# Kernel optimization log

Hardware: AMD Instinct MI355X
Metric: run time of the kernel (lower is better)

## Reference

```python
import jax, jax.numpy as jnp
import numpy as np

VOCAB, D, PAD, SPARSITY = 6, 32, 5, 0.15


def setup_inputs() -> dict:
    key = jax.random.key(0)
    ks = jax.random.split(key, 16)
    x = jax.random.randint(ks[0], (256, 4096), 0, VOCAB, dtype=jnp.int32)
    s = 0.1
    emb = jax.random.normal(ks[1], (VOCAB, D), jnp.float32) * s
    return {
        "x": x,
        "emb": emb,
        # selector: D -> D//2 -> 1 (sigmoid)
        "sel_w1": jax.random.normal(ks[2], (D, D // 2), jnp.float32) * s,
        "sel_b1": jnp.zeros((D // 2,), jnp.float32),
        "sel_w2": jax.random.normal(ks[3], (D // 2, 1), jnp.float32) * s,
        "sel_b2": jnp.zeros((1,), jnp.float32),
        # approximator: D -> D -> D
        "app_w1": jax.random.normal(ks[4], (D, D), jnp.float32) * s,
        "app_b1": jnp.zeros((D,), jnp.float32),
        "app_w2": jax.random.normal(ks[5], (D, D), jnp.float32) * s,
        "app_b2": jnp.zeros((D,), jnp.float32),
        # classifier: D -> D//2 -> 1 (sigmoid)
        "cls_w1": jax.random.normal(ks[6], (D, D // 2), jnp.float32) * s,
        "cls_b1": jnp.zeros((D // 2,), jnp.float32),
        "cls_w2": jax.random.normal(ks[7], (D // 2, 1), jnp.float32) * s,
        "cls_b2": jnp.zeros((1,), jnp.float32),
    }


def reference(x, emb, sel_w1, sel_b1, sel_w2, sel_b2,
              app_w1, app_b1, app_w2, app_b2,
              cls_w1, cls_b1, cls_w2, cls_b2):
    B, S = x.shape
    k = max(1, int(S * SPARSITY))
    table = emb.at[PAD].set(0.0)            # padding_idx row is zero
    e = table[x]                            # [B, S, D]
    # selector scores (tiny MLP + sigmoid)
    h = jax.nn.relu(e @ sel_w1 + sel_b1)
    scores = jax.nn.sigmoid((h @ sel_w2 + sel_b2).squeeze(-1))  # [B, S]
    _, top_idx = jax.lax.top_k(scores, k)   # [B, k]
    sel = jnp.take_along_axis(e, top_idx[..., None], axis=1)    # [B, k, D]
    a = jax.nn.relu(sel @ app_w1 + app_b1) @ app_w2 + app_b2    # [B, k, D]
    pooled = a.mean(axis=1)                 # [B, D]
    c = jax.nn.relu(pooled @ cls_w1 + cls_b1)
    pred = jax.nn.sigmoid((c @ cls_w2 + cls_b2).squeeze(-1))    # [B]
    return pred, top_idx, scores
```

## Files before the change

kernel.cpp:

```cpp
#include <hip/hip_runtime.h>
#include <math.h>

#define VOCABN 6
#define DIM 32
#define PADI 5
#define BATCH 256
#define SEQ 4096
#define KSEL 614

__device__ __forceinline__ int mbcnt64(unsigned long long m) {
    return __builtin_amdgcn_mbcnt_hi((unsigned)(m >> 32),
           __builtin_amdgcn_mbcnt_lo((unsigned)m, 0u));
}

__device__ __forceinline__ float lut6(float s0, float s1, float s2, float s3,
                                      float s4, float s5, int tk) {
    float r = s0;
    r = (tk == 1) ? s1 : r;
    r = (tk == 2) ? s2 : r;
    r = (tk == 3) ? s3 : r;
    r = (tk == 4) ? s4 : r;
    r = (tk == 5) ? s5 : r;
    return r;
}

__global__ __launch_bounds__(1024) void fused_row_kernel(
    const int* __restrict__ x,
    const float* __restrict__ emb,
    const float* __restrict__ sel_w1, const float* __restrict__ sel_b1,
    const float* __restrict__ sel_w2, const float* __restrict__ sel_b2,
    const float* __restrict__ app_w1, const float* __restrict__ app_b1,
    const float* __restrict__ app_w2, const float* __restrict__ app_b2,
    const float* __restrict__ cls_w1, const float* __restrict__ cls_b1,
    const float* __restrict__ cls_w2, const float* __restrict__ cls_b2,
    float* __restrict__ out_pred,
    float* __restrict__ out_topidx,
    float* __restrict__ out_scores) {
    const int b = blockIdx.x;
    const int t = threadIdx.x;
    const int lane = t & 63;
    const int w = t >> 6;

    __shared__ float s_emb[VOCABN * DIM];
    __shared__ float s_selw1[DIM * (DIM / 2)];
    __shared__ float s_selb1[DIM / 2], s_selw2[DIM / 2];
    __shared__ float s_selb2, s_clsb2v;
    __shared__ float s_appw1[DIM * DIM];
    __shared__ float s_appw2[DIM * DIM];
    __shared__ float s_appb1[DIM], s_appb2[DIM];
    __shared__ float s_clsw1[DIM * (DIM / 2)];
    __shared__ float s_clsb1[DIM / 2], s_clsw2[DIM / 2];
    __shared__ float s_ah[VOCABN * DIM];
    __shared__ __align__(16) float s_score[8];
    __shared__ __align__(16) int s_wtot[16][8];
    __shared__ __align__(16) int s_wpre[16][8];
    __shared__ __align__(16) int s_selbase[8];

    const int4 tw = *(const int4*)(x + (size_t)b * SEQ + t * 4);

    s_appw1[t] = app_w1[t];
    s_appw2[t] = app_w2[t];
    if (t < 512) s_selw1[t] = sel_w1[t];
    else s_clsw1[t - 512] = cls_w1[t - 512];
    if (t < 192) s_emb[t] = (t >= PADI * DIM) ? 0.f : emb[t];
    else if (t < 208) { int i = t - 192; s_selb1[i] = sel_b1[i]; }
    else if (t < 224) { int i = t - 208; s_selw2[i] = sel_w2[i]; }
    else if (t < 256) { int i = t - 224; s_appb1[i] = app_b1[i]; }
    else if (t < 288) { int i = t - 256; s_appb2[i] = app_b2[i]; }
    else if (t < 304) { int i = t - 288; s_clsb1[i] = cls_b1[i]; }
    else if (t < 320) { int i = t - 304; s_clsw2[i] = cls_w2[i]; }
    else if (t == 320) s_selb2 = sel_b2[0];
    else if (t == 321) s_clsb2v = cls_b2[0];

    int tok[4];
    tok[0] = tw.x; tok[1] = tw.y; tok[2] = tw.z; tok[3] = tw.w;

    unsigned long long msk[VOCABN][4];
    #pragma unroll
    for (int v = 0; v < VOCABN; ++v) {
        #pragma unroll
        for (int i = 0; i < 4; ++i) msk[v][i] = __ballot(tok[i] == v);
    }
    if (lane == 0) {
        int c[VOCABN];
        #pragma unroll
        for (int v = 0; v < VOCABN; ++v)
            c[v] = __popcll(msk[v][0]) + __popcll(msk[v][1]) +
                   __popcll(msk[v][2]) + __popcll(msk[v][3]);
        *(int4*)&s_wtot[w][0] = make_int4(c[0], c[1], c[2], c[3]);
        *(int2*)&s_wtot[w][4] = make_int2(c[4], c[5]);
    }

    __syncthreads();

    if (w == 0) {
        int sv = lane >> 3; if (sv >= VOCABN) sv -= VOCABN;
        const int j0 = (lane & 7) * 2;
        const float2 bj = *(const float2*)(s_selb1 + j0);
        const float2 wj = *(const float2*)(s_selw2 + j0);
        float h0 = bj.x, h1 = bj.y;
        #pragma unroll
        for (int d = 0; d < DIM; ++d) {
            const float e = s_emb[sv * DIM + d];
            const float2 ww = *(const float2*)(s_selw1 + d * (DIM / 2) + j0);
            h0 += e * ww.x;
            h1 += e * ww.y;
        }
        float part = fmaxf(h0, 0.f) * wj.x + fmaxf(h1, 0.f) * wj.y;
        part += __shfl_xor(part, 1, 64);
        part += __shfl_xor(part, 2, 64);
        part += __shfl_xor(part, 4, 64);
        const float sig = 1.f / (1.f + expf(-(part + s_selb2)));
        float scv[VOCABN];
        #pragma unroll
        for (int v = 0; v < VOCABN; ++v) scv[v] = __shfl(sig, v * 8, 64);
        if (lane < VOCABN) s_score[lane] = scv[lane];

        int tv[VOCABN];
        #pragma unroll
        for (int v = 0; v < VOCABN; ++v) tv[v] = s_wtot[lane & 15][v];
        #pragma unroll
        for (int m = 1; m <= 8; m <<= 1) {
            #pragma unroll
            for (int v = 0; v < VOCABN; ++v) tv[v] += __shfl_xor(tv[v], m, 64);
        }
        int rk[VOCABN];
        #pragma unroll
        for (int v = 0; v < VOCABN; ++v) {
            int r = 0;
            #pragma unroll
            for (int u = 0; u < VOCABN; ++u) {
                if (scv[u] > scv[v]) ++r;
                else if (scv[u] == scv[v] && u < v) ++r;
            }
            rk[v] = r;
        }
        if (lane < VOCABN) {
            const int v = lane;
            int before = 0;
            #pragma unroll
            for (int u = 0; u < VOCABN; ++u) before += (rk[u] < rk[v]) ? tv[u] : 0;
            const int base = before < KSEL ? before : KSEL;
            int take = KSEL - base;
            take = tv[v] < take ? tv[v] : take;
            take = take > 0 ? take : 0;
            s_selbase[v] = take | (base << 16);
        }
    } else if (w == 1) {
        int tv[VOCABN], inc[VOCABN];
        #pragma unroll
        for (int v = 0; v < VOCABN; ++v) { tv[v] = s_wtot[lane & 15][v]; inc[v] = tv[v]; }
        #pragma unroll
        for (int off = 1; off <= 8; off <<= 1) {
            #pragma unroll
            for (int v = 0; v < VOCABN; ++v) {
                int up = __shfl_up(inc[v], off, 64);
                if ((lane & 15) >= off) inc[v] += up;
            }
        }
        if (lane < 16) {
            *(int4*)&s_wpre[lane][0] = make_int4(inc[0] - tv[0], inc[1] - tv[1],
                                                 inc[2] - tv[2], inc[3] - tv[3]);
            *(int2*)&s_wpre[lane][4] = make_int2(inc[4] - tv[4], inc[5] - tv[5]);
        }
    } else if (w >= 2 && w < 5) {
        const int i = t - 128, v = i >> 5, j = i & 31;
        float acc = s_appb1[j];
        #pragma unroll
        for (int d = 0; d < DIM; ++d) acc += s_emb[v * DIM + d] * s_appw1[d * DIM + j];
        s_ah[i] = fmaxf(acc, 0.f);
    }

    __syncthreads();

    {
        const float4 s03 = *(const float4*)&s_score[0];
        const float2 s45 = *(const float2*)&s_score[4];
        float4 f;
        f.x = lut6(s03.x, s03.y, s03.z, s03.w, s45.x, s45.y, tok[0]);
        f.y = lut6(s03.x, s03.y, s03.z, s03.w, s45.x, s45.y, tok[1]);
        f.z = lut6(s03.x, s03.y, s03.z, s03.w, s45.x, s45.y, tok[2]);
        f.w = lut6(s03.x, s03.y, s03.z, s03.w, s45.x, s45.y, tok[3]);
        *(float4*)(out_scores + (size_t)b * SEQ + t * 4) = f;
    }

    {
        const int4 wp03 = *(const int4*)&s_wpre[w][0];
        const int2 wp45 = *(const int2*)&s_wpre[w][4];
        const int4 sb03 = *(const int4*)&s_selbase[0];
        const int2 sb45 = *(const int2*)&s_selbase[4];
        const int wp[VOCABN] = {wp03.x, wp03.y, wp03.z, wp03.w, wp45.x, wp45.y};
        const int sb[VOCABN] = {sb03.x, sb03.y, sb03.z, sb03.w, sb45.x, sb45.y};
        #pragma unroll
        for (int v = 0; v < VOCABN; ++v) {
            const int sel = sb[v] & 0xffff;
            const int bs = sb[v] >> 16;
            int p = wp[v] + mbcnt64(msk[v][0]) + mbcnt64(msk[v][1]) +
                    mbcnt64(msk[v][2]) + mbcnt64(msk[v][3]);
            #pragma unroll
            for (int i = 0; i < 4; ++i) {
                if (tok[i] == v) {
                    if (p < sel) out_topidx[(size_t)b * KSEL + bs + p] = (float)(t * 4 + i);
                    ++p;
                }
            }
        }
    }

    if (w == 5) {
        const int4 sb03 = *(const int4*)&s_selbase[0];
        const int2 sb45 = *(const int2*)&s_selbase[4];
        const int sel6[VOCABN] = {sb03.x & 0xffff, sb03.y & 0xffff, sb03.z & 0xffff,
                                  sb03.w & 0xffff, sb45.x & 0xffff, sb45.y & 0xffff};
        const int j = lane & 31;
        const int half = lane >> 5;
        float part = 0.f;
        #pragma unroll
        for (int r = 0; r < 3; ++r) {
            const int v = 2 * r + half;
            float av = s_appb2[j];
            #pragma unroll
            for (int k = 0; k < DIM; ++k) av += s_ah[v * DIM + k] * s_appw2[k * DIM + j];
            part += (float)sel6[v] * av;
        }
        float pooled = (part + __shfl_xor(part, 32, 64)) * (1.f / (float)KSEL);
        float c = (lane < DIM / 2) ? s_clsb1[lane] : 0.f;
        #pragma unroll
        for (int d = 0; d < DIM; ++d) {
            const float pd = __shfl(pooled, d, 64);
            if (lane < DIM / 2) c += pd * s_clsw1[d * (DIM / 2) + lane];
        }
        float term = (lane < DIM / 2) ? fmaxf(c, 0.f) * s_clsw2[lane] : 0.f;
        term += __shfl_xor(term, 1, 64);
        term += __shfl_xor(term, 2, 64);
        term += __shfl_xor(term, 4, 64);
        term += __shfl_xor(term, 8, 64);
        if (lane == 0) out_pred[b] = 1.f / (1.f + expf(-(term + s_clsb2v)));
    }
}

extern "C" void kernel_launch(void* const* d_in, const int* in_sizes, int n_in,
                              void* d_out, int out_size, void* d_ws, size_t ws_size,
                              hipStream_t stream) {
    const int*   x      = (const int*)  d_in[0];
    const float* emb    = (const float*)d_in[1];
    const float* sel_w1 = (const float*)d_in[2];
    const float* sel_b1 = (const float*)d_in[3];
    const float* sel_w2 = (const float*)d_in[4];
    const float* sel_b2 = (const float*)d_in[5];
    const float* app_w1 = (const float*)d_in[6];
    const float* app_b1 = (const float*)d_in[7];
    const float* app_w2 = (const float*)d_in[8];
    const float* app_b2 = (const float*)d_in[9];
    const float* cls_w1 = (const float*)d_in[10];
    const float* cls_b1 = (const float*)d_in[11];
    const float* cls_w2 = (const float*)d_in[12];
    const float* cls_b2 = (const float*)d_in[13];

    float* out = (float*)d_out;
    float* out_pred   = out;
    float* out_topidx = out + BATCH;
    float* out_scores = out + BATCH + BATCH * KSEL;

    fused_row_kernel<<<BATCH, 1024, 0, stream>>>(
        x, emb, sel_w1, sel_b1, sel_w2, sel_b2,
        app_w1, app_b1, app_w2, app_b2,
        cls_w1, cls_b1, cls_w2, cls_b2,
        out_pred, out_topidx, out_scores);
}
```

Baseline: 88.06 us.

## Compute selector scores from global memory before the first barrier

```diff
diff --git a/kernel.cpp b/kernel.cpp
--- a/kernel.cpp
+++ b/kernel.cpp
@@ -42,14 +42,12 @@
     const int w = t >> 6;
 
     __shared__ float s_emb[VOCABN * DIM];
-    __shared__ float s_selw1[DIM * (DIM / 2)];
-    __shared__ float s_selb1[DIM / 2], s_selw2[DIM / 2];
-    __shared__ float s_selb2, s_clsb2v;
     __shared__ float s_appw1[DIM * DIM];
     __shared__ float s_appw2[DIM * DIM];
     __shared__ float s_appb1[DIM], s_appb2[DIM];
     __shared__ float s_clsw1[DIM * (DIM / 2)];
     __shared__ float s_clsb1[DIM / 2], s_clsw2[DIM / 2];
+    __shared__ float s_clsb2v;
     __shared__ float s_ah[VOCABN * DIM];
     __shared__ __align__(16) float s_score[8];
     __shared__ __align__(16) int s_wtot[16][8];
@@ -60,20 +58,46 @@
 
     s_appw1[t] = app_w1[t];
     s_appw2[t] = app_w2[t];
-    if (t < 512) s_selw1[t] = sel_w1[t];
-    else s_clsw1[t - 512] = cls_w1[t - 512];
-    if (t < 192) s_emb[t] = (t >= PADI * DIM) ? 0.f : emb[t];
-    else if (t < 208) { int i = t - 192; s_selb1[i] = sel_b1[i]; }
-    else if (t < 224) { int i = t - 208; s_selw2[i] = sel_w2[i]; }
-    else if (t < 256) { int i = t - 224; s_appb1[i] = app_b1[i]; }
-    else if (t < 288) { int i = t - 256; s_appb2[i] = app_b2[i]; }
-    else if (t < 304) { int i = t - 288; s_clsb1[i] = cls_b1[i]; }
-    else if (t < 320) { int i = t - 304; s_clsw2[i] = cls_w2[i]; }
-    else if (t == 320) s_selb2 = sel_b2[0];
-    else if (t == 321) s_clsb2v = cls_b2[0];
+    if (t >= 512 && t < 1024) s_clsw1[t - 512] = cls_w1[t - 512];
+    if (t >= 192 && t < 384) { int i = t - 192; s_emb[i] = (i >= PADI * DIM) ? 0.f : emb[i]; }
+    else if (t < 416 && t >= 384) { int i = t - 384; s_appb1[i] = app_b1[i]; }
+    else if (t < 448 && t >= 416) { int i = t - 416; s_appb2[i] = app_b2[i]; }
+    else if (t < 464 && t >= 448) { int i = t - 448; s_clsb1[i] = cls_b1[i]; }
+    else if (t < 480 && t >= 464) { int i = t - 464; s_clsw2[i] = cls_w2[i]; }
+    else if (t == 480) s_clsb2v = cls_b2[0];
 
     int tok[4];
     tok[0] = tw.x; tok[1] = tw.y; tok[2] = tw.z; tok[3] = tw.w;
+
+    float scv[VOCABN];
+    if (w == 0) {
+        int sv = lane >> 3; if (sv >= VOCABN) sv -= VOCABN;
+        const int j0 = (lane & 7) * 2;
+        const float2 bj = *(const float2*)(sel_b1 + j0);
+        const float2 wj = *(const float2*)(sel_w2 + j0);
+        float h0 = bj.x, h1 = bj.y;
+        if (sv != PADI) {
+            const float4* e4 = (const float4*)(emb + sv * DIM);
+            #pragma unroll
+            for (int q = 0; q < 8; ++q) {
+                const float4 e = e4[q];
+                const float2 wa = *(const float2*)(sel_w1 + (q * 4 + 0) * (DIM / 2) + j0);
+                const float2 wb = *(const float2*)(sel_w1 + (q * 4 + 1) * (DIM / 2) + j0);
+                const float2 wc = *(const float2*)(sel_w1 + (q * 4 + 2) * (DIM / 2) + j0);
+                const float2 wd = *(const float2*)(sel_w1 + (q * 4 + 3) * (DIM / 2) + j0);
+                h0 += e.x * wa.x + e.y * wb.x + e.z * wc.x + e.w * wd.x;
+                h1 += e.x * wa.y + e.y * wb.y + e.z * wc.y + e.w * wd.y;
+            }
+        }
+        float part = fmaxf(h0, 0.f) * wj.x + fmaxf(h1, 0.f) * wj.y;
+        part += __shfl_xor(part, 1, 64);
+        part += __shfl_xor(part, 2, 64);
+        part += __shfl_xor(part, 4, 64);
+        const float sig = 1.f / (1.f + expf(-(part + sel_b2[0])));
+        #pragma unroll
+        for (int v = 0; v < VOCABN; ++v) scv[v] = __shfl(sig, v * 8, 64);
+        if (lane < VOCABN) s_score[lane] = scv[lane];
+    }
 
     unsigned long long msk[VOCABN][4];
     #pragma unroll
@@ -89,86 +113,6 @@
                    __popcll(msk[v][2]) + __popcll(msk[v][3]);
         *(int4*)&s_wtot[w][0] = make_int4(c[0], c[1], c[2], c[3]);
         *(int2*)&s_wtot[w][4] = make_int2(c[4], c[5]);
-    }
-
-    __syncthreads();
-
-    if (w == 0) {
-        int sv = lane >> 3; if (sv >= VOCABN) sv -= VOCABN;
-        const int j0 = (lane & 7) * 2;
-        const float2 bj = *(const float2*)(s_selb1 + j0);
-        const float2 wj = *(const float2*)(s_selw2 + j0);
-        float h0 = bj.x, h1 = bj.y;
-        #pragma unroll
-        for (int d = 0; d < DIM; ++d) {
-            const float e = s_emb[sv * DIM + d];
-            const float2 ww = *(const float2*)(s_selw1 + d * (DIM / 2) + j0);
-            h0 += e * ww.x;
-            h1 += e * ww.y;
-        }
-        float part = fmaxf(h0, 0.f) * wj.x + fmaxf(h1, 0.f) * wj.y;
-        part += __shfl_xor(part, 1, 64);
-        part += __shfl_xor(part, 2, 64);
-        part += __shfl_xor(part, 4, 64);
-        const float sig = 1.f / (1.f + expf(-(part + s_selb2)));
-        float scv[VOCABN];
-        #pragma unroll
-        for (int v = 0; v < VOCABN; ++v) scv[v] = __shfl(sig, v * 8, 64);
-        if (lane < VOCABN) s_score[lane] = scv[lane];
-
-        int tv[VOCABN];
-        #pragma unroll
-        for (int v = 0; v < VOCABN; ++v) tv[v] = s_wtot[lane & 15][v];
-        #pragma unroll
-        for (int m = 1; m <= 8; m <<= 1) {
-            #pragma unroll
-            for (int v = 0; v < VOCABN; ++v) tv[v] += __shfl_xor(tv[v], m, 64);
-        }
-        int rk[VOCABN];
-        #pragma unroll
-        for (int v = 0; v < VOCABN; ++v) {
-            int r = 0;
-            #pragma unroll
-            for (int u = 0; u < VOCABN; ++u) {
-                if (scv[u] > scv[v]) ++r;
-                else if (scv[u] == scv[v] && u < v) ++r;
-            }
-            rk[v] = r;
-        }
-        if (lane < VOCABN) {
-            const int v = lane;
-            int before = 0;
-            #pragma unroll
-            for (int u = 0; u < VOCABN; ++u) before += (rk[u] < rk[v]) ? tv[u] : 0;
-            const int base = before < KSEL ? before : KSEL;
-            int take = KSEL - base;
-            take = tv[v] < take ? tv[v] : take;
-            take = take > 0 ? take : 0;
-            s_selbase[v] = take | (base << 16);
-        }
-    } else if (w == 1) {
-        int tv[VOCABN], inc[VOCABN];
-        #pragma unroll
-        for (int v = 0; v < VOCABN; ++v) { tv[v] = s_wtot[lane & 15][v]; inc[v] = tv[v]; }
-        #pragma unroll
-        for (int off = 1; off <= 8; off <<= 1) {
-            #pragma unroll
-            for (int v = 0; v < VOCABN; ++v) {
-                int up = __shfl_up(inc[v], off, 64);
-                if ((lane & 15) >= off) inc[v] += up;
-            }
-        }
-        if (lane < 16) {
-            *(int4*)&s_wpre[lane][0] = make_int4(inc[0] - tv[0], inc[1] - tv[1],
-                                                 inc[2] - tv[2], inc[3] - tv[3]);
-            *(int2*)&s_wpre[lane][4] = make_int2(inc[4] - tv[4], inc[5] - tv[5]);
-        }
-    } else if (w >= 2 && w < 5) {
-        const int i = t - 128, v = i >> 5, j = i & 31;
-        float acc = s_appb1[j];
-        #pragma unroll
-        for (int d = 0; d < DIM; ++d) acc += s_emb[v * DIM + d] * s_appw1[d * DIM + j];
-        s_ah[i] = fmaxf(acc, 0.f);
     }
 
     __syncthreads();
@@ -183,6 +127,64 @@
         f.w = lut6(s03.x, s03.y, s03.z, s03.w, s45.x, s45.y, tok[3]);
         *(float4*)(out_scores + (size_t)b * SEQ + t * 4) = f;
     }
+
+    if (w == 0) {
+        int tv[VOCABN];
+        #pragma unroll
+        for (int v = 0; v < VOCABN; ++v) tv[v] = s_wtot[lane & 15][v];
+        #pragma unroll
+        for (int m = 1; m <= 8; m <<= 1) {
+            #pragma unroll
+            for (int v = 0; v < VOCABN; ++v) tv[v] += __shfl_xor(tv[v], m, 64);
+        }
+        int rk[VOCABN];
+        #pragma unroll
+        for (int v = 0; v < VOCABN; ++v) {
+            int r = 0;
+            #pragma unroll
+            for (int u = 0; u < VOCABN; ++u) {
+                if (scv[u] > scv[v]) ++r;
+                else if (scv[u] == scv[v] && u < v) ++r;
+            }
+            rk[v] = r;
+        }
+        if (lane < VOCABN) {
+            const int v = lane;
+            int before = 0;
+            #pragma unroll
+            for (int u = 0; u < VOCABN; ++u) before += (rk[u] < rk[v]) ? tv[u] : 0;
+            const int base = before < KSEL ? before : KSEL;
+            int take = KSEL - base;
+            take = tv[v] < take ? tv[v] : take;
+            take = take > 0 ? take : 0;
+            s_selbase[v] = take | (base << 16);
+        }
+    } else if (w == 1) {
+        int tv[VOCABN], inc[VOCABN];
+        #pragma unroll
+        for (int v = 0; v < VOCABN; ++v) { tv[v] = s_wtot[lane & 15][v]; inc[v] = tv[v]; }
+        #pragma unroll
+        for (int off = 1; off <= 8; off <<= 1) {
+            #pragma unroll
+            for (int v = 0; v < VOCABN; ++v) {
+                int up = __shfl_up(inc[v], off, 64);
+                if ((lane & 15) >= off) inc[v] += up;
+            }
+        }
+        if (lane < 16) {
+            *(int4*)&s_wpre[lane][0] = make_int4(inc[0] - tv[0], inc[1] - tv[1],
+                                                 inc[2] - tv[2], inc[3] - tv[3]);
+            *(int2*)&s_wpre[lane][4] = make_int2(inc[4] - tv[4], inc[5] - tv[5]);
+        }
+    } else if (w >= 2 && w < 5) {
+        const int i = t - 128, v = i >> 5, j = i & 31;
+        float acc = s_appb1[j];
+        #pragma unroll
+        for (int d = 0; d < DIM; ++d) acc += s_emb[v * DIM + d] * s_appw1[d * DIM + j];
+        s_ah[i] = fmaxf(acc, 0.f);
+    }
+
+    __syncthreads();
 
     {
         const int4 wp03 = *(const int4*)&s_wpre[w][0];
```

New measurement: 88.71 us. Within noise of the previous version (+0.7%).
